# Performance work log

Measured on AMD Instinct MI355X. Metric: run time of the kernel, lower is better.

Reference implementation:

```python
import jax, jax.numpy as jnp
import numpy as np

HEADS = 4
HEAD_DIM = 128  # GATConv out_channels
NEG_SLOPE_ATT = 0.2   # GATConv internal leaky relu
NEG_SLOPE_ACT = 0.01  # nn.LeakyReLU() default


def gat_conv(x, edge_index, W, att_src, att_dst, bias):
    # x: [N, F]; edge_index: [2, E] (row 0 = src j, row 1 = dst i)
    N = x.shape[0]
    h = (x @ W).reshape(N, HEADS, HEAD_DIM)            # [N, H, C]
    loops = jnp.arange(N, dtype=edge_index.dtype)
    src = jnp.concatenate([edge_index[0], loops])      # add self loops
    dst = jnp.concatenate([edge_index[1], loops])
    a_src = jnp.einsum('nhc,hc->nh', h, att_src)       # [N, H]
    a_dst = jnp.einsum('nhc,hc->nh', h, att_dst)
    e = jax.nn.leaky_relu(a_src[src] + a_dst[dst], NEG_SLOPE_ATT)  # [E', H]
    # segment softmax over incoming edges of each dst node
    emax = jax.ops.segment_max(e, dst, num_segments=N)
    ex = jnp.exp(e - emax[dst])
    denom = jax.ops.segment_sum(ex, dst, num_segments=N)
    alpha = ex / (denom[dst] + 1e-16)                  # [E', H]
    msg = h[src] * alpha[:, :, None]                   # [E', H, C]
    out = jax.ops.segment_sum(msg, dst, num_segments=N)
    return out.reshape(N, HEADS * HEAD_DIM) + bias     # [N, H*C]


def branch(x, edge_index, W, att_src, att_dst, bias, fc1_w, fc1_b):
    h = gat_conv(x, edge_index, W, att_src, att_dst, bias)
    h = jax.nn.leaky_relu(h, NEG_SLOPE_ACT)
    g = jnp.mean(h, axis=0, keepdims=True)             # global mean pool, batch all zeros -> [1, H*C]
    g = jax.nn.leaky_relu(g @ fc1_w + fc1_b, NEG_SLOPE_ACT)
    return g  # dropout is identity in eval mode


def setup_inputs() -> dict:
    key = jax.random.key(0)
    ks = jax.random.split(key, 10)
    N, E, F = 20000, 320000, 512
    HC = HEADS * HEAD_DIM
    s = 1.0 / np.sqrt(F)
    return {
        'x': jax.random.normal(ks[0], (N, F), jnp.float32),
        'adj': jax.random.randint(ks[1], (2, E), 0, N, jnp.int64),
        'wt_x': jax.random.normal(ks[2], (N, F), jnp.float32),
        'wt_adj': jax.random.randint(ks[3], (2, E), 0, N, jnp.int64),
        'W': jax.random.normal(ks[4], (F, HC), jnp.float32) * s,
        'att_src': jax.random.normal(ks[5], (HEADS, HEAD_DIM), jnp.float32) * s,
        'att_dst': jax.random.normal(ks[6], (HEADS, HEAD_DIM), jnp.float32) * s,
        'bias': jnp.zeros((HC,), jnp.float32),
        'fc1_w': jax.random.normal(ks[7], (HC, 512), jnp.float32) * (1.0 / np.sqrt(HC)),
        'fc1_b': jnp.zeros((512,), jnp.float32),
    }


def reference(x, adj, wt_x, wt_adj, W, att_src, att_dst, bias, fc1_w, fc1_b):
    g = branch(x, adj, W, att_src, att_dst, bias, fc1_w, fc1_b)
    wt_g = branch(wt_x, wt_adj, W, att_src, att_dst, bias, fc1_w, fc1_b)
    xd = g - wt_g
    return jnp.concatenate([g, wt_g, xd], axis=1)  # [1, 3*512]
```

## Files before the change

kernel.cpp:

```cpp
#include <hip/hip_runtime.h>
#include <hip/hip_bf16.h>

typedef unsigned short u16;
typedef short bf16x8 __attribute__((ext_vector_type(8)));
typedef float f32x4 __attribute__((ext_vector_type(4)));
typedef float f32x2 __attribute__((ext_vector_type(2)));

__device__ __forceinline__ u16 f2b(float f) {
    unsigned x = __float_as_uint(f);
    return (u16)((x + 0x7fffu + ((x >> 16) & 1u)) >> 16);
}

__device__ __forceinline__ int pkbf(float lo, float hi) {
    return __builtin_amdgcn_perm(__float_as_uint(hi), __float_as_uint(lo), 0x07060302);
}

__device__ __forceinline__ void pkfma(f32x2& acc, f32x2 f, f32x2 ex) {
    asm("v_pk_fma_f32 %0, %1, %2, %0" : "+v"(acc) : "v"(f), "v"(ex));
}

__global__ __launch_bounds__(256) void castwt_count(
    const float* __restrict__ W, u16* __restrict__ Wt,
    const int* __restrict__ adj, const int* __restrict__ wadj,
    int E, int Mpad, int* __restrict__ deg) {
    __shared__ u16 tile[64][65];
    if (blockIdx.x < 64) {
        int tx = threadIdx.x & 63, ty = threadIdx.x >> 6;
        int bx = blockIdx.x & 7, by = blockIdx.x >> 3;
#pragma unroll
        for (int r = 0; r < 16; ++r) {
            int row = ty + (r << 2);
            tile[tx][row] = f2b(W[(by * 64 + row) * 512 + bx * 64 + tx]);
        }
        __syncthreads();
#pragma unroll
        for (int r = 0; r < 16; ++r) {
            int row = ty + (r << 2);
            Wt[(bx * 64 + row) * 512 + by * 64 + tx] = tile[row][tx];
        }
    } else {
        int i = (blockIdx.x - 64) * 256 + threadIdx.x;
        if (i < 2 * E) {
            int d = (i < E) ? adj[E + i] : (wadj[E + (i - E)] + Mpad);
            atomicAdd(&deg[d], 1);
        }
    }
}

__global__ __launch_bounds__(256, 2) void gemm_scatter(
    const float* __restrict__ xA, const float* __restrict__ xW, const u16* __restrict__ Bt,
    unsigned char* __restrict__ h8, const float* __restrict__ att_src,
    const float* __restrict__ att_dst, float* __restrict__ asrc, float* __restrict__ adst,
    int N, int Mpad, int gemmB,
    const int* __restrict__ adj, const int* __restrict__ wadj, int E,
    int* __restrict__ cursor, int* __restrict__ csrc) {
    __shared__ float lA[2][64 * 32];
    __shared__ u16 lB[2][512 * 32];
    if (blockIdx.x >= gemmB) {
        int i = (blockIdx.x - gemmB) * 256 + threadIdx.x;
        if (i < 2 * E) {
            int s, d;
            if (i < E) {
                s = adj[i];
                d = adj[E + i];
            } else {
                s = wadj[i - E] + Mpad;
                d = wadj[E + (i - E)] + Mpad;
            }
            int p = atomicAdd(&cursor[d], 1);
            csrc[p] = s;
        }
        return;
    }
    const int tid = threadIdx.x;
    const int w = tid >> 6, l = tid & 63;
    const int row0 = blockIdx.x * 64;
    const int head = w;
    const int mlane = l & 15, quad = l >> 4;
    const int R2v = 2 * Mpad;

    const float* src = (row0 >= Mpad) ? xW : xA;
    const int rbase = row0 - (row0 >= Mpad ? Mpad : 0);
    const int arow = (l >> 3);
    const int acol = (((l & 7) ^ arow) << 2);
    const int brow = (l >> 2);
    const int bcol = (((l & 3) ^ ((l >> 3) & 3)) << 3);

    auto stage = [&](int b, int k0) {
#pragma unroll
        for (int g = 0; g < 2; ++g) {
            int lrow = rbase + (w << 4) + (g << 3) + arow;
            lrow = min(lrow, N - 1);
            const float* ga = src + (size_t)lrow * 512 + k0 + acol;
            float* la = &lA[b][((w << 4) + (g << 3)) << 5];
            __builtin_amdgcn_global_load_lds((const __attribute__((address_space(1))) void*)ga,
                                             (__attribute__((address_space(3))) void*)la, 16, 0, 0);
        }
#pragma unroll
        for (int s = 0; s < 8; ++s) {
            const u16* gb = Bt + (size_t)((w << 7) + (s << 4) + brow) * 512 + (k0 + bcol);
            u16* lb = &lB[b][((w << 7) + (s << 4)) << 5];
            __builtin_amdgcn_global_load_lds((const __attribute__((address_space(1))) void*)gb,
                                             (__attribute__((address_space(3))) void*)lb, 16, 0, 0);
        }
    };

    f32x4 acc[4][8];
#pragma unroll
    for (int i = 0; i < 4; i++)
#pragma unroll
        for (int j = 0; j < 8; j++) acc[i][j] = f32x4{0.f, 0.f, 0.f, 0.f};

    stage(0, 0);
    __syncthreads();
    int cur = 0;
    for (int t = 0; t < 16; ++t) {
        if (t < 15) stage(cur ^ 1, (t + 1) << 5);
        bf16x8 af[4], bfr[8];
#pragma unroll
        for (int i = 0; i < 4; i++) {
            const float* rb = &lA[cur][(i * 16 + mlane) * 32];
            float4 f0 = *(const float4*)(rb + (((quad * 2) ^ (mlane & 7)) << 2));
            float4 f1 = *(const float4*)(rb + (((quad * 2 + 1) ^ (mlane & 7)) << 2));
            int* ai = (int*)&af[i];
            ai[0] = pkbf(f0.x, f0.y);
            ai[1] = pkbf(f0.z, f0.w);
            ai[2] = pkbf(f1.x, f1.y);
            ai[3] = pkbf(f1.z, f1.w);
        }
#pragma unroll
        for (int j = 0; j < 8; j++)
            bfr[j] = *(const bf16x8*)&lB[cur][((w << 7) + j * 16 + mlane) * 32 +
                                             ((quad ^ ((mlane >> 1) & 3)) << 3)];
#pragma unroll
        for (int i = 0; i < 4; i++)
#pragma unroll
            for (int j = 0; j < 8; j++)
                acc[i][j] = __builtin_amdgcn_mfma_f32_16x16x32_bf16(af[i], bfr[j], acc[i][j], 0, 0, 0);
        __syncthreads();
        cur ^= 1;
    }

    float as_j[8], ad_j[8];
#pragma unroll
    for (int j = 0; j < 8; j++) {
        as_j[j] = att_src[(head << 7) + j * 16 + mlane];
        ad_j[j] = att_dst[(head << 7) + j * 16 + mlane];
    }
#pragma unroll
    for (int i = 0; i < 4; i++) {
#pragma unroll
        for (int r = 0; r < 4; r++) {
            float vs = 0.f, vd = 0.f;
#pragma unroll
            for (int j = 0; j < 8; j++) {
                float hv = acc[i][j][r];
                vs += hv * as_j[j];
                vd += hv * ad_j[j];
            }
#pragma unroll
            for (int o = 8; o >= 1; o >>= 1) {
                vs += __shfl_xor(vs, o);
                vd += __shfl_xor(vd, o);
            }
            if (mlane == 0) {
                int rg = row0 + i * 16 + quad * 4 + r;
                asrc[head * R2v + rg] = vs;
                adst[head * R2v + rg] = vd;
            }
        }
    }

    unsigned char* hstage = (unsigned char*)&lB[0][0];
#pragma unroll
    for (int i = 0; i < 4; i++)
#pragma unroll
        for (int j = 0; j < 8; j++)
#pragma unroll
            for (int r = 0; r < 4; r++) {
                int row = i * 16 + quad * 4 + r;
                int colb = (w << 7) + j * 16 + mlane;
                float v = acc[i][j][r];
                unsigned pk = __builtin_amdgcn_cvt_pk_fp8_f32(v, v, 0, false);
                hstage[row * 512 + (colb ^ ((row & 7) << 4))] = (unsigned char)(pk & 0xff);
            }
    __syncthreads();
#pragma unroll
    for (int k = 0; k < 8; ++k) {
        int c = (k << 8) + tid;
        int hd = c >> 9;
        int rem = c & 511;
        int row = rem >> 3;
        int cch = rem & 7;
        int lofs = row * 512 + ((((hd << 7) + (cch << 4))) ^ ((row & 7) << 4));
        int4 v = *(const int4*)&hstage[lofs];
        *(int4*)&h8[(((size_t)(hd * R2v + row0 + row)) << 7) + (cch << 4)] = v;
    }
}

__global__ __launch_bounds__(256) void scanA(const int* __restrict__ deg, int* __restrict__ off,
                                             int* __restrict__ bsum, int n, int N, int Mpad) {
    __shared__ int wsum[4];
    int tid = threadIdx.x, lane = tid & 63, wid = tid >> 6;
    int i = blockIdx.x * 256 + tid;
    int valid = (i < N) || (i >= Mpad && i < Mpad + N);
    int d = (i < n) ? deg[i] + (valid ? 1 : 0) : 0;
    int x = d;
#pragma unroll
    for (int o = 1; o < 64; o <<= 1) {
        int y = __shfl_up(x, (unsigned)o, 64);
        if (lane >= o) x += y;
    }
    if (lane == 63) wsum[wid] = x;
    __syncthreads();
    int woff = 0;
    for (int j = 0; j < wid; ++j) woff += wsum[j];
    if (i < n) off[i] = woff + x - d;
    if (tid == 255) bsum[blockIdx.x] = woff + x;
}

__global__ __launch_bounds__(256) void scanB(const int* __restrict__ bsum, int* __restrict__ bbase,
                                             int nb, int* __restrict__ off, int n) {
    __shared__ int wsum[4];
    int tid = threadIdx.x, lane = tid & 63, wid = tid >> 6;
    int d = (tid < nb) ? bsum[tid] : 0;
    int x = d;
#pragma unroll
    for (int o = 1; o < 64; o <<= 1) {
        int y = __shfl_up(x, (unsigned)o, 64);
        if (lane >= o) x += y;
    }
    if (lane == 63) wsum[wid] = x;
    __syncthreads();
    int woff = 0;
    for (int j = 0; j < wid; ++j) woff += wsum[j];
    int excl = woff + x - d;
    if (tid < nb) bbase[tid] = excl;
    if (tid == nb - 1) off[n] = excl + d;
}

__global__ void scanC(int* __restrict__ off, const int* __restrict__ bbase,
                      int* __restrict__ cursor, int* __restrict__ csrc, int n, int N, int Mpad) {
    int i = blockIdx.x * blockDim.x + threadIdx.x;
    if (i < n) {
        int o = off[i] + bbase[i >> 8];
        off[i] = o;
        int valid = (i < N) || (i >= Mpad && i < Mpad + N);
        if (valid) csrc[o] = i;
        cursor[i] = o + valid;
    }
}

__global__ __launch_bounds__(256, 6) void gat_aggregate13(
    const unsigned char* __restrict__ h8, const float* __restrict__ asrc,
    const float* __restrict__ adst, const int* __restrict__ off, const int* __restrict__ csrc,
    const float* __restrict__ bias, float* __restrict__ partAB, int Mpad) {
    const int R2 = 2 * Mpad;
    __shared__ float spool[128];
    int tid = threadIdx.x;
    if (tid < 128) spool[tid] = 0.f;
    __syncthreads();
    const int wv = tid >> 6, l = tid & 63;
    const int gi = (l >> 3) & 3;
    const int hi = l >> 5;
    const int chb = (l & 7) << 4;
    const int head = (blockIdx.x & 7) >> 1;
    const int gc = blockIdx.x & 1;
    const unsigned char* h8h = h8 + (((size_t)head * R2) << 7);
    const float* ash = asrc + (size_t)head * R2;
    const float* adh = adst + (size_t)head * R2;
    float bb[16];
#pragma unroll
    for (int k = 0; k < 16; ++k) bb[k] = bias[head * 128 + chb + k];
    float pool[16];
#pragma unroll
    for (int k = 0; k < 16; ++k) pool[k] = 0.f;

    const int hb = gc * Mpad;
    const int half = Mpad >> 1;
    int widx = ((blockIdx.x >> 3) << 2) + wv;
    const int cstride = gridDim.x >> 1;

    for (int p = widx; p < half; p += cstride) {
        int d0 = (p << 1) + hb;
        int q0 = off[d0], q1 = off[d0 + 1], q2 = off[d0 + 2];
        int n0 = q1 - q0, n1 = q2 - q1;
        int nmax = max(n0, n1);
        if (nmax == 0) continue;
        int nm = hi ? n1 : n0;
        int qm = hi ? q1 : q0;
        float ad = adh[d0 + hi];
        f32x2 acc2[8];
#pragma unroll
        for (int j = 0; j < 8; ++j) acc2[j] = f32x2{0.f, 0.f};
        float dsum = 0.f;

        int i0 = gi, i1 = 4 + gi, i2 = 8 + gi, i3 = 12 + gi;
        int E0 = csrc[qm + ((i0 < nm) ? i0 : 0)];
        int E1 = csrc[qm + ((i1 < nm) ? i1 : 0)];
        int E2 = csrc[qm + ((i2 < nm) ? i2 : 0)];
        int E3 = csrc[qm + ((i3 < nm) ? i3 : 0)];
        float A0 = ash[E0];
        int4 H0 = *(const int4*)(h8h + (((size_t)E0) << 7) + chb);
        float A1 = ash[E1];
        int4 H1 = *(const int4*)(h8h + (((size_t)E1) << 7) + chb);

#pragma unroll 2
        for (int base = 0; base < nmax; base += 4) {
            int i4 = base + 16 + gi;
            int E4 = csrc[qm + ((i4 < nm) ? i4 : 0)];
            float A2 = ash[E2];
            int4 H2 = *(const int4*)(h8h + (((size_t)E2) << 7) + chb);
            float e = A0 + ad;
            float em = fmaxf(e, 0.2f * e);
            float ex = __expf(em);
            ex = ((base + gi) < nm) ? ex : 0.f;
            dsum += ex;
            f32x2 exv = {ex, ex};
            f32x2 f;
            f = __builtin_amdgcn_cvt_pk_f32_fp8(H0.x, false); pkfma(acc2[0], f, exv);
            f = __builtin_amdgcn_cvt_pk_f32_fp8(H0.x, true);  pkfma(acc2[1], f, exv);
            f = __builtin_amdgcn_cvt_pk_f32_fp8(H0.y, false); pkfma(acc2[2], f, exv);
            f = __builtin_amdgcn_cvt_pk_f32_fp8(H0.y, true);  pkfma(acc2[3], f, exv);
            f = __builtin_amdgcn_cvt_pk_f32_fp8(H0.z, false); pkfma(acc2[4], f, exv);
            f = __builtin_amdgcn_cvt_pk_f32_fp8(H0.z, true);  pkfma(acc2[5], f, exv);
            f = __builtin_amdgcn_cvt_pk_f32_fp8(H0.w, false); pkfma(acc2[6], f, exv);
            f = __builtin_amdgcn_cvt_pk_f32_fp8(H0.w, true);  pkfma(acc2[7], f, exv);
            A0 = A1; H0 = H1;
            A1 = A2; H1 = H2;
            E2 = E3; E3 = E4;
        }
        dsum += __shfl_xor(dsum, 8);
        dsum += __shfl_xor(dsum, 16);
#pragma unroll
        for (int j = 0; j < 8; ++j) {
            acc2[j].x += __shfl_xor(acc2[j].x, 8);
            acc2[j].y += __shfl_xor(acc2[j].y, 8);
            acc2[j].x += __shfl_xor(acc2[j].x, 16);
            acc2[j].y += __shfl_xor(acc2[j].y, 16);
        }
        if (nm > 0) {
            float inv = 1.f / (dsum + 1e-16f);
#pragma unroll
            for (int j = 0; j < 8; ++j) {
                float o0 = acc2[j].x * inv + bb[2 * j];
                float o1 = acc2[j].y * inv + bb[2 * j + 1];
                pool[2 * j] += fmaxf(o0, 0.01f * o0);
                pool[2 * j + 1] += fmaxf(o1, 0.01f * o1);
            }
        }
    }
    if ((l & 31) < 8) {
#pragma unroll
        for (int k = 0; k < 16; ++k) atomicAdd(&spool[chb + k], pool[k]);
    }
    __syncthreads();
    if (tid < 128) {
        int slot = (blockIdx.x >> 3) & 63;
        float* dp = partAB + (gc ? 64 * 512 : 0) + (slot << 9) + head * 128 + tid;
        atomicAdd(dp, spool[tid]);
    }
}

__global__ __launch_bounds__(256) void fc_final2(
    const float* __restrict__ partAB, const float* __restrict__ w, const float* __restrict__ b,
    float* __restrict__ out, float invN) {
    __shared__ float gA[512], gB[512];
    __shared__ float rA[256], rB[256];
    int t = threadIdx.x;
    for (int i = t; i < 512; i += 256) {
        float sA = 0.f, sB = 0.f;
        for (int r = 0; r < 64; ++r) {
            sA += partAB[r * 512 + i];
            sB += partAB[64 * 512 + r * 512 + i];
        }
        gA[i] = sA * invN;
        gB[i] = sB * invN;
    }
    __syncthreads();
    int jj = t & 31, ks = t >> 5;
    int j = blockIdx.x * 32 + jj;
    float sA = 0.f, sB = 0.f;
    for (int k = ks * 64; k < ks * 64 + 64; ++k) {
        float wv = w[k * 512 + j];
        sA += gA[k] * wv;
        sB += gB[k] * wv;
    }
    rA[t] = sA;
    rB[t] = sB;
    __syncthreads();
    if (ks == 0) {
#pragma unroll
        for (int s2 = 1; s2 < 8; ++s2) {
            sA += rA[jj + 32 * s2];
            sB += rB[jj + 32 * s2];
        }
        sA += b[j];
        sB += b[j];
        sA = sA >= 0.f ? sA : 0.01f * sA;
        sB = sB >= 0.f ? sB : 0.01f * sB;
        out[j] = sA;
        out[512 + j] = sB;
        out[1024 + j] = sA - sB;
    }
}

extern "C" void kernel_launch(void* const* d_in, const int* in_sizes, int n_in,
                              void* d_out, int out_size, void* d_ws, size_t ws_size,
                              hipStream_t stream) {
    const float* x = (const float*)d_in[0];
    const int* adj = (const int*)d_in[1];
    const float* wtx = (const float*)d_in[2];
    const int* wadj = (const int*)d_in[3];
    const float* W = (const float*)d_in[4];
    const float* att_s = (const float*)d_in[5];
    const float* att_d = (const float*)d_in[6];
    const float* bias = (const float*)d_in[7];
    const float* fc1w = (const float*)d_in[8];
    const float* fc1b = (const float*)d_in[9];
    float* out = (float*)d_out;

    const int N = in_sizes[0] / 512;
    const int E = in_sizes[1] / 2;
    const int Mpad = ((N + 127) / 128) * 128;
    const int R2 = 2 * Mpad;
    const int nb = (R2 + 255) / 256;
    const int eb = (2 * E + 255) / 256;

    char* p = (char*)d_ws;
    auto alloc = [&](size_t bytes) -> char* {
        char* r = p;
        p += (bytes + 255) & ~(size_t)255;
        return r;
    };
    unsigned char* h8 = (unsigned char*)alloc((size_t)R2 * 512);
    u16* Wt = (u16*)alloc(512 * 512 * 2);
    float* asrc = (float*)alloc((size_t)R2 * 4 * 4);
    float* adst = (float*)alloc((size_t)R2 * 4 * 4);
    int* deg = (int*)alloc((size_t)R2 * 4);
    int* off = (int*)alloc((size_t)(R2 + 1) * 4);
    int* cursor = (int*)alloc((size_t)R2 * 4);
    int* bsum = (int*)alloc(256 * 4);
    int* bbase = (int*)alloc(256 * 4);
    int* csrc = (int*)alloc((size_t)2 * (E + N) * 4);
    float* partAB = (float*)alloc((size_t)2 * 64 * 512 * 4);

    hipMemsetAsync(partAB, 0, (size_t)2 * 64 * 512 * 4, stream);
    hipMemsetAsync(deg, 0, (size_t)R2 * 4, stream);

    castwt_count<<<64 + eb, 256, 0, stream>>>(W, Wt, adj, wadj, E, Mpad, deg);

    scanA<<<nb, 256, 0, stream>>>(deg, off, bsum, R2, N, Mpad);
    scanB<<<1, 256, 0, stream>>>(bsum, bbase, nb, off, R2);
    scanC<<<nb, 256, 0, stream>>>(off, bbase, cursor, csrc, R2, N, Mpad);

    gemm_scatter<<<R2 / 64 + eb, 256, 0, stream>>>(x, wtx, Wt, h8, att_s, att_d, asrc, adst,
                                                   N, Mpad, R2 / 64, adj, wadj, E, cursor, csrc);

    gat_aggregate13<<<1536, 256, 0, stream>>>(h8, asrc, adst, off, csrc, bias, partAB, Mpad);

    fc_final2<<<16, 256, 0, stream>>>(partAB, fc1w, fc1b, out, 1.0f / (float)N);
}
```

Before: 308.1 us.

## Replace three-kernel scan with single-pass decoupled-lookback scan and fold memset

Replaces the three scan kernels (block scan, block-sum scan, fixup) with one kernel that uses dynamic block IDs and decoupled look-back through a global status array. The partAB zeroing and the status-array reset move into the castwt_count kernel, which removes one memset. This cuts three launches and one memset down to one launch, lowering launch and serialization overhead. In exchange it adds serial spin-waiting on predecessor blocks, which stays small with only about 157 blocks.

New measurement: 310.8 us. Within noise of the previous version (+0.9%).

```diff
diff --git a/kernel.cpp b/kernel.cpp
--- a/kernel.cpp
+++ b/kernel.cpp
@@ -22,8 +22,12 @@
 __global__ __launch_bounds__(256) void castwt_count(
     const float* __restrict__ W, u16* __restrict__ Wt,
     const int* __restrict__ adj, const int* __restrict__ wadj,
-    int E, int Mpad, int* __restrict__ deg) {
+    int E, int Mpad, int* __restrict__ deg,
+    float* __restrict__ partAB, unsigned int* __restrict__ state) {
     __shared__ u16 tile[64][65];
+    int gid = blockIdx.x * 256 + threadIdx.x;
+    if (gid < 2 * 64 * 512) partAB[gid] = 0.f;
+    if (blockIdx.x == gridDim.x - 1) state[threadIdx.x] = 0u;
     if (blockIdx.x < 64) {
         int tx = threadIdx.x & 63, ty = threadIdx.x >> 6;
         int bx = blockIdx.x & 7, by = blockIdx.x >> 3;
@@ -45,6 +49,60 @@
             atomicAdd(&deg[d], 1);
         }
     }
+}
+
+__global__ __launch_bounds__(256) void scan_onepass(
+    const int* __restrict__ deg, int* __restrict__ off, int* __restrict__ cursor,
+    int* __restrict__ csrc, unsigned int* __restrict__ state, int n, int N, int Mpad) {
+    __shared__ int wsum[4];
+    __shared__ int sbid_s, prefix_s;
+    const int tid = threadIdx.x, lane = tid & 63, wid = tid >> 6;
+    if (tid == 0) sbid_s = (int)atomicAdd(&state[192], 1u);
+    __syncthreads();
+    const int sbid = sbid_s;
+    const int i = sbid * 256 + tid;
+    int valid = (i < N) || (i >= Mpad && i < Mpad + N);
+    int d = (i < n) ? deg[i] + valid : 0;
+    int x = d;
+#pragma unroll
+    for (int o = 1; o < 64; o <<= 1) {
+        int y = __shfl_up(x, (unsigned)o, 64);
+        if (lane >= o) x += y;
+    }
+    if (lane == 63) wsum[wid] = x;
+    __syncthreads();
+    int woff = 0;
+    for (int j = 0; j < wid; ++j) woff += wsum[j];
+    const int lexcl = woff + x - d;
+    int tot = 0;
+#pragma unroll
+    for (int j = 0; j < 4; ++j) tot += wsum[j];
+    if (tid == 0) {
+        int pfx = 0;
+        if (sbid == 0) {
+            atomicExch(&state[0], (2u << 30) | (unsigned)tot);
+        } else {
+            atomicExch(&state[sbid], (1u << 30) | (unsigned)tot);
+            int j = sbid - 1;
+            for (;;) {
+                unsigned v;
+                do { v = atomicAdd(&state[j], 0u); } while (v == 0u);
+                pfx += (int)(v & 0x3FFFFFFFu);
+                if ((v >> 30) == 2u) break;
+                --j;
+            }
+            atomicExch(&state[sbid], (2u << 30) | (unsigned)(pfx + tot));
+        }
+        prefix_s = pfx;
+    }
+    __syncthreads();
+    const int o = prefix_s + lexcl;
+    if (i < n) {
+        off[i] = o;
+        cursor[i] = o + valid;
+        if (valid) csrc[o] = i;
+    }
+    if (i == n - 1) off[n] = o + d;
 }
 
 __global__ __launch_bounds__(256, 2) void gemm_scatter(
@@ -195,59 +253,6 @@
         int lofs = row * 512 + ((((hd << 7) + (cch << 4))) ^ ((row & 7) << 4));
         int4 v = *(const int4*)&hstage[lofs];
         *(int4*)&h8[(((size_t)(hd * R2v + row0 + row)) << 7) + (cch << 4)] = v;
-    }
-}
-
-__global__ __launch_bounds__(256) void scanA(const int* __restrict__ deg, int* __restrict__ off,
-                                             int* __restrict__ bsum, int n, int N, int Mpad) {
-    __shared__ int wsum[4];
-    int tid = threadIdx.x, lane = tid & 63, wid = tid >> 6;
-    int i = blockIdx.x * 256 + tid;
-    int valid = (i < N) || (i >= Mpad && i < Mpad + N);
-    int d = (i < n) ? deg[i] + (valid ? 1 : 0) : 0;
-    int x = d;
-#pragma unroll
-    for (int o = 1; o < 64; o <<= 1) {
-        int y = __shfl_up(x, (unsigned)o, 64);
-        if (lane >= o) x += y;
-    }
-    if (lane == 63) wsum[wid] = x;
-    __syncthreads();
-    int woff = 0;
-    for (int j = 0; j < wid; ++j) woff += wsum[j];
-    if (i < n) off[i] = woff + x - d;
-    if (tid == 255) bsum[blockIdx.x] = woff + x;
-}
-
-__global__ __launch_bounds__(256) void scanB(const int* __restrict__ bsum, int* __restrict__ bbase,
-                                             int nb, int* __restrict__ off, int n) {
-    __shared__ int wsum[4];
-    int tid = threadIdx.x, lane = tid & 63, wid = tid >> 6;
-    int d = (tid < nb) ? bsum[tid] : 0;
-    int x = d;
-#pragma unroll
-    for (int o = 1; o < 64; o <<= 1) {
-        int y = __shfl_up(x, (unsigned)o, 64);
-        if (lane >= o) x += y;
-    }
-    if (lane == 63) wsum[wid] = x;
-    __syncthreads();
-    int woff = 0;
-    for (int j = 0; j < wid; ++j) woff += wsum[j];
-    int excl = woff + x - d;
-    if (tid < nb) bbase[tid] = excl;
-    if (tid == nb - 1) off[n] = excl + d;
-}
-
-__global__ void scanC(int* __restrict__ off, const int* __restrict__ bbase,
-                      int* __restrict__ cursor, int* __restrict__ csrc, int n, int N, int Mpad) {
-    int i = blockIdx.x * blockDim.x + threadIdx.x;
-    if (i < n) {
-        int o = off[i] + bbase[i >> 8];
-        off[i] = o;
-        int valid = (i < N) || (i >= Mpad && i < Mpad + N);
-        if (valid) csrc[o] = i;
-        cursor[i] = o + valid;
     }
 }
 
@@ -440,19 +445,15 @@
     int* deg = (int*)alloc((size_t)R2 * 4);
     int* off = (int*)alloc((size_t)(R2 + 1) * 4);
     int* cursor = (int*)alloc((size_t)R2 * 4);
-    int* bsum = (int*)alloc(256 * 4);
-    int* bbase = (int*)alloc(256 * 4);
+    unsigned int* state = (unsigned int*)alloc(256 * 4);
     int* csrc = (int*)alloc((size_t)2 * (E + N) * 4);
     float* partAB = (float*)alloc((size_t)2 * 64 * 512 * 4);
 
-    hipMemsetAsync(partAB, 0, (size_t)2 * 64 * 512 * 4, stream);
     hipMemsetAsync(deg, 0, (size_t)R2 * 4, stream);
 
-    castwt_count<<<64 + eb, 256, 0, stream>>>(W, Wt, adj, wadj, E, Mpad, deg);
-
-    scanA<<<nb, 256, 0, stream>>>(deg, off, bsum, R2, N, Mpad);
-    scanB<<<1, 256, 0, stream>>>(bsum, bbase, nb, off, R2);
-    scanC<<<nb, 256, 0, stream>>>(off, bbase, cursor, csrc, R2, N, Mpad);
+    castwt_count<<<64 + eb, 256, 0, stream>>>(W, Wt, adj, wadj, E, Mpad, deg, partAB, state);
+
+    scan_onepass<<<nb, 256, 0, stream>>>(deg, off, cursor, csrc, state, R2, N, Mpad);
 
     gemm_scatter<<<R2 / 64 + eb, 256, 0, stream>>>(x, wtx, Wt, h8, att_s, att_d, asrc, adst,
                                                    N, Mpad, R2 / 64, adj, wadj, E, cursor, csrc);
```
